# Optimization experiments

Measured on AMD Instinct MI355X. Metric: run time of the kernel, lower is better.

Reference implementation:

```python
import jax, jax.numpy as jnp
import numpy as np
from jax import lax

B, C, H, W = 16, 384, 28, 28
HEADS = 8


def _ln(x, g, b):
    mu = jnp.mean(x, axis=-1, keepdims=True)
    var = jnp.var(x, axis=-1, keepdims=True)
    return (x - mu) * lax.rsqrt(var + 1e-5) * g + b


def setup_inputs() -> dict:
    key = jax.random.key(0)
    ks = jax.random.split(key, 8)
    s = 0.02
    return {
        "cls_token": jax.random.normal(ks[0], (B, 1, C), dtype=jnp.float32),
        "x": jax.random.normal(ks[1], (B, C, H, W), dtype=jnp.float32),
        "conv_w": jax.random.normal(ks[2], (C, 1, 3, 3), dtype=jnp.float32) * s,
        "conv_b": jnp.zeros((C,), jnp.float32),
        "ln1_g": jnp.ones((C,), jnp.float32),
        "ln1_b": jnp.zeros((C,), jnp.float32),
        "qkv_w": jax.random.normal(ks[3], (3 * C, C), dtype=jnp.float32) * s,
        "proj_w": jax.random.normal(ks[4], (C, C), dtype=jnp.float32) * s,
        "proj_b": jnp.zeros((C,), jnp.float32),
        "ln2_g": jnp.ones((C,), jnp.float32),
        "ln2_b": jnp.zeros((C,), jnp.float32),
        "fc1_w": jax.random.normal(ks[5], (4 * C, C), dtype=jnp.float32) * s,
        "fc1_b": jnp.zeros((4 * C,), jnp.float32),
        "fc2_w": jax.random.normal(ks[6], (C, 4 * C), dtype=jnp.float32) * s,
        "fc2_b": jnp.zeros((C,), jnp.float32),
    }


def reference(cls_token, x, conv_w, conv_b, ln1_g, ln1_b, qkv_w, proj_w, proj_b,
              ln2_g, ln2_b, fc1_w, fc1_b, fc2_w, fc2_b):
    Bv, Cv, Hv, Wv = x.shape
    h = HEADS
    d = Cv // h
    # depthwise 3x3 positional conv (groups=dim), residual add
    pe = lax.conv_general_dilated(
        x, conv_w, window_strides=(1, 1), padding="SAME",
        feature_group_count=Cv,
        dimension_numbers=("NCHW", "OIHW", "NCHW")) + conv_b[None, :, None, None]
    x = x + pe
    x_patch = x.reshape(Bv, Cv, Hv * Wv).transpose(0, 2, 1)  # [B, HW, C]
    xc = jnp.concatenate([cls_token, x_patch], axis=1)       # [B, N, C]
    N = xc.shape[1]

    # --- Attention with inline global_attn stats (first-call / int sentinel path) ---
    y = _ln(xc, ln1_g, ln1_b)
    qkv = (y @ qkv_w.T).reshape(Bv, N, 3, h, d)
    q = qkv[:, :, 0].transpose(0, 2, 1, 3)  # [B, h, N, d]
    k = qkv[:, :, 1].transpose(0, 2, 1, 3)
    v = qkv[:, :, 2].transpose(0, 2, 1, 3)
    scale = d ** -0.5
    attn = jax.nn.softmax(jnp.einsum("bhnd,bhmd->bhnm", q, k) * scale, axis=-1)
    # per-token global attention statistic: mean over heads of cls row (excl. cls)
    global_attn = jnp.mean(attn[:, :, 0, 1:], axis=1)  # [B, N-1]
    o = jnp.einsum("bhnm,bhmd->bhnd", attn, v).transpose(0, 2, 1, 3).reshape(Bv, N, Cv)
    xc = xc + (o @ proj_w.T + proj_b)

    # --- MLP (GELU exact, matching torch nn.GELU default) ---
    y2 = _ln(xc, ln2_g, ln2_b)
    m = jax.nn.gelu(y2 @ fc1_w.T + fc1_b, approximate=False) @ fc2_w.T + fc2_b
    xc = xc + m

    cls_out = xc[:, :1]                                            # [B, 1, C]
    x_out = xc[:, 1:].transpose(0, 2, 1).reshape(Bv, Cv, Hv, Wv)    # [B, C, H, W]
    return cls_out, x_out, global_attn
```

## Files before the change

kernel.cpp:

```cpp
#include <hip/hip_runtime.h>
#include <hip/hip_bf16.h>

#define DI __device__ __forceinline__

typedef __attribute__((ext_vector_type(4))) float f32x4;
typedef __attribute__((ext_vector_type(8))) short bf16x8;
typedef __attribute__((ext_vector_type(4))) short bf16x4;

static constexpr int CB = 16;
static constexpr int CC = 384;
static constexpr int CH = 28, CW = 28;
static constexpr int CD = 48;
static constexpr int CN = 785;
static constexpr int CM = CB * CN;
static constexpr int C3 = 3 * CC;
static constexpr int CF = 4 * CC;
static constexpr int HW = CH * CW;
static constexpr int NP = 832;

DI short f2b(float f) {
  __hip_bfloat16 h = __float2bfloat16(f);
  return *reinterpret_cast<short*>(&h);
}
DI float b2f(short s) {
  union { unsigned u; float f; } x;
  x.u = ((unsigned)(unsigned short)s) << 16;
  return x.f;
}

DI void gload16(const short* g, short* l) {
  __builtin_amdgcn_global_load_lds((const __attribute__((address_space(1))) void*)g,
                                   (__attribute__((address_space(3))) void*)l, 16, 0, 0);
}

__global__ void k_misc(const float* __restrict__ cls, float* __restrict__ xc,
                       float* __restrict__ ga) {
  const int gid = blockIdx.x * 256 + threadIdx.x;
  if (gid < CB * HW) ga[gid] = 0.f;
  if (gid < CB * CC) {
    const int b = gid / CC, c = gid % CC;
    xc[((size_t)b * CN) * CC + c] = cls[gid];
  }
}

__global__ void k_wconv(const float* __restrict__ s0, const float* __restrict__ s1,
                        const float* __restrict__ s2, const float* __restrict__ s3,
                        short* __restrict__ dst) {
  const int gid = (blockIdx.x * 256 + threadIdx.x) * 4;
  if (gid >= 1769472) return;
  const float* s; int off;
  if (gid < 442368)       { s = s0; off = gid; }
  else if (gid < 589824)  { s = s1; off = gid - 442368; }
  else if (gid < 1179648) { s = s2; off = gid - 589824; }
  else                    { s = s3; off = gid - 1179648; }
  f32x4 v = *(const f32x4*)(s + off);
  bf16x4 o;
#pragma unroll
  for (int i = 0; i < 4; i++) o[i] = f2b(v[i]);
  *(bf16x4*)(dst + gid) = o;
}

__global__ __launch_bounds__(256) void k_conv_t(const float* __restrict__ x,
                                                const float* __restrict__ cw,
                                                const float* __restrict__ cb,
                                                float* __restrict__ xc) {
  __shared__ float T[64][65];
  __shared__ float Wc[64 * 9];
  __shared__ float Cbs[64];
  const int b = blockIdx.z;
  const int cc = blockIdx.y * 64;
  const int hw0 = blockIdx.x * 64;
  const int t = threadIdx.x;
  const int hwi = t & 63, ci0 = t >> 6;
  const int hw = hw0 + hwi;
  const int yy = hw / CW, xx = hw % CW;
  const int ci2 = t & 63, hb2 = t >> 6;

  for (int i = t; i < 64 * 9; i += 256) Wc[i] = cw[cc * 9 + i];
  if (t < 64) Cbs[t] = cb[cc + t];
  __syncthreads();
  if (hw < HW) {
#pragma unroll
    for (int j = 0; j < 16; j++) {
      const int cl = ci0 * 16 + j;
      const float* xp = x + ((size_t)(b * CC + cc + cl)) * HW;
      float acc = Cbs[cl];
      const float center = xp[yy * CW + xx];
#pragma unroll
      for (int ky = 0; ky < 3; ky++) {
        const int iy = yy + ky - 1;
        if (iy < 0 || iy >= CH) continue;
#pragma unroll
        for (int kx = 0; kx < 3; kx++) {
          const int ix = xx + kx - 1;
          if (ix < 0 || ix >= CW) continue;
          acc += Wc[cl * 9 + ky * 3 + kx] * xp[iy * CW + ix];
        }
      }
      T[cl][hwi] = center + acc;
    }
  }
  __syncthreads();
#pragma unroll
  for (int j = 0; j < 16; j++) {
    const int hwl = hb2 + j * 4;
    if (hw0 + hwl < HW)
      xc[((size_t)b * CN + 1 + hw0 + hwl) * CC + cc + ci2] = T[ci2][hwl];
  }
}

__global__ __launch_bounds__(256) void k_ln(const float* __restrict__ xin,
                                            const float* __restrict__ g,
                                            const float* __restrict__ bta,
                                            short* __restrict__ y, int Mtot) {
  const int row = blockIdx.x * 4 + (threadIdx.x >> 6);
  const int l = threadIdx.x & 63;
  if (row >= Mtot) return;
  const float* xr = xin + (size_t)row * CC;
  float v[6], s = 0.f, ss = 0.f;
#pragma unroll
  for (int i = 0; i < 6; i++) {
    v[i] = xr[l + i * 64];
    s += v[i];
    ss += v[i] * v[i];
  }
#pragma unroll
  for (int m = 1; m < 64; m <<= 1) { s += __shfl_xor(s, m); ss += __shfl_xor(ss, m); }
  const float mu = s * (1.f / CC);
  const float var = ss * (1.f / CC) - mu * mu;
  const float r = rsqrtf(var + 1e-5f);
#pragma unroll
  for (int i = 0; i < 6; i++) {
    const int c = l + i * 64;
    y[(size_t)row * CC + c] = f2b((v[i] - mu) * r * g[c] + bta[c]);
  }
}

template <int BM, int DOGELU, int DORES, int DOBIAS, int OUTBF>
__global__ __launch_bounds__(256) void k_gemm(const short* __restrict__ A,
                                              const short* __restrict__ W,
                                              const float* __restrict__ bias,
                                              const float* __restrict__ resid,
                                              void* __restrict__ out_,
                                              int M, int N, int K) {
  constexpr int MI = BM / 32;
  constexpr int ACALLS = BM / 64;
  __shared__ short As[2 * BM * 32];
  __shared__ short Bs[2 * 128 * 32];
  const int bm = blockIdx.x * BM, bn = blockIdx.y * 128;
  const int t = threadIdx.x, w = t >> 6, l = t & 63, g = l >> 4, li = l & 15;
  const int wm = (w >> 1) * (BM / 2), wn = (w & 1) * 64;

  const int srow = l >> 2;
  const int scol = (l & 3) * 8;
  const short* aSrc[ACALLS]; int aOff[ACALLS];
#pragma unroll
  for (int j = 0; j < ACALLS; j++) {
    int arow = bm + w * (BM / 4) + j * 16 + srow; if (arow > M - 1) arow = M - 1;
    aSrc[j] = A + (size_t)arow * K + scol;
    aOff[j] = (w * (BM / 4) + j * 16) * 32;
  }
  const short* bSrc[2]; int bOff[2];
#pragma unroll
  for (int j = 0; j < 2; j++) {
    const int brow = bn + w * 32 + j * 16 + srow;
    bSrc[j] = W + (size_t)brow * K + scol;
    bOff[j] = (w * 32 + j * 16) * 32;
  }

  auto stage = [&](int buf, int kt) {
    const int ko = kt * 32;
#pragma unroll
    for (int j = 0; j < ACALLS; j++)
      gload16(aSrc[j] + ko, &As[buf * (BM * 32)] + aOff[j]);
#pragma unroll
    for (int j = 0; j < 2; j++)
      gload16(bSrc[j] + ko, &Bs[buf * (128 * 32)] + bOff[j]);
  };

  f32x4 acc[MI][4] = {};
  const int nkt = K / 32;
  stage(0, 0);
  __syncthreads();
  int cur = 0;
  for (int kt = 0; kt < nkt; kt++) {
    if (kt + 1 < nkt) stage(cur ^ 1, kt + 1);
    const short* Ab = &As[cur * (BM * 32)];
    const short* Bb = &Bs[cur * (128 * 32)];
    bf16x8 af[MI], bf[4];
#pragma unroll
    for (int mi = 0; mi < MI; mi++)
      af[mi] = *(const bf16x8*)&Ab[(wm + mi * 16 + li) * 32 + g * 8];
#pragma unroll
    for (int ni = 0; ni < 4; ni++)
      bf[ni] = *(const bf16x8*)&Bb[(wn + ni * 16 + li) * 32 + g * 8];
#pragma unroll
    for (int mi = 0; mi < MI; mi++)
#pragma unroll
      for (int ni = 0; ni < 4; ni++)
        acc[mi][ni] = __builtin_amdgcn_mfma_f32_16x16x32_bf16(af[mi], bf[ni], acc[mi][ni], 0, 0, 0);
    __syncthreads();
    cur ^= 1;
  }

#pragma unroll
  for (int mi = 0; mi < MI; mi++)
#pragma unroll
    for (int ni = 0; ni < 4; ni++) {
      const int col = bn + wn + ni * 16 + li;
      float bv = 0.f;
      if constexpr (DOBIAS) bv = bias[col];
#pragma unroll
      for (int r = 0; r < 4; r++) {
        const int row = bm + wm + mi * 16 + g * 4 + r;
        if (row < M) {
          float v = acc[mi][ni][r] + bv;
          if constexpr (DOGELU) v = 0.5f * v * (1.f + erff(v * 0.7071067811865475f));
          if constexpr (DORES) v += resid[(size_t)row * N + col];
          if constexpr (OUTBF)
            ((short*)out_)[(size_t)row * N + col] = f2b(v);
          else
            ((float*)out_)[(size_t)row * N + col] = v;
        }
      }
    }
}

__global__ __launch_bounds__(256) void k_vt(const short* __restrict__ qkv,
                                            short* __restrict__ vt) {
  __shared__ short Tl[48 * 71];
  const int n0 = blockIdx.x * 64;
  const int bh = blockIdx.y;
  const int b = bh >> 3, h = bh & 7;
  const int t = threadIdx.x;
  const size_t bbase = (size_t)b * CN;
#pragma unroll
  for (int it = 0; it < 2; it++) {
    const int gi = t + it * 256;
    if (gi < 384) {
      const int nrel = gi / 6, dg = gi % 6;
      const int n = n0 + nrel;
      bf16x8 val = {};
      if (n < CN)
        val = *(const bf16x8*)(qkv + (bbase + n) * C3 + 2 * CC + h * CD + dg * 8);
#pragma unroll
      for (int i = 0; i < 8; i++) Tl[(dg * 8 + i) * 71 + nrel] = val[i];
    }
  }
  __syncthreads();
#pragma unroll
  for (int it = 0; it < 2; it++) {
    const int gj = t + it * 256;
    if (gj < 384) {
      const int d = gj >> 3, ng = gj & 7;
      bf16x8 v;
#pragma unroll
      for (int i = 0; i < 8; i++) v[i] = Tl[d * 71 + ng * 8 + i];
      *(bf16x8*)(vt + ((size_t)bh * CD + d) * NP + n0 + ng * 8) = v;
    }
  }
}

__global__ __launch_bounds__(256) void k_attn(const short* __restrict__ qkv,
                                              const short* __restrict__ vt,
                                              short* __restrict__ o) {
  __shared__ short Ks[64 * 48];
  __shared__ short Vs[48 * 64];
  const int f = blockIdx.x;
  const int xslot = f & 7, grp = f >> 3;
  const int bh = xslot + 8 * (grp & 15);
  const int qt = grp >> 4;
  const int b = bh >> 3, h = bh & 7;
  const int q0 = qt * 64;
  const int t = threadIdx.x, w = t >> 6, l = t & 63, g = l >> 4, li = l & 15;
  const size_t bbase = (size_t)b * CN;

  const int qrow = q0 + w * 16 + li;
  const int qr = qrow > CN - 1 ? CN - 1 : qrow;
  const short* qb = qkv + (bbase + qr) * C3 + h * CD;
  bf16x8 qf0 = *(const bf16x8*)(qb + g * 8);
  bf16x8 qf1 = {};
  if (g < 2) qf1 = *(const bf16x8*)(qb + 32 + g * 8);

  float mr = -1e30f, ls = 0.f;
  f32x4 oa[3] = {};
  const float scale = 0.14433756729740643f;

  const int krow0 = t / 6, kcg0 = t % 6;
  const int krow1 = (t + 256) / 6, kcg1 = (t + 256) % 6;
  const int vd0 = t >> 3, vkvg0 = t & 7;
  const int vd1 = (t + 256) >> 3, vkvg1 = (t + 256) & 7;
  const short* kbase = qkv + bbase * C3 + CC + h * CD;
  const short* vbase = vt + (size_t)bh * CD * NP;

  bf16x8 kr0 = {}, kr1 = {}, vr0 = {}, vr1 = {};
  kr0 = *(const bf16x8*)(kbase + (size_t)min(krow0, CN - 1) * C3 + kcg0 * 8);
  vr0 = *(const bf16x8*)(vbase + vd0 * NP + vkvg0 * 8);
  if (t < 128) {
    kr1 = *(const bf16x8*)(kbase + (size_t)min(krow1, CN - 1) * C3 + kcg1 * 8);
    vr1 = *(const bf16x8*)(vbase + vd1 * NP + vkvg1 * 8);
  }

  for (int kt = 0; kt < 13; kt++) {
    const int kv0 = kt * 64;
    __syncthreads();
    *(bf16x8*)((char*)Ks + ((krow0 * 96 + kcg0 * 16) ^ ((krow0 & 7) << 4))) = kr0;
    *(bf16x8*)((char*)Vs + ((vd0 * 128 + vkvg0 * 16) ^ ((vd0 & 7) << 4))) = vr0;
    if (t < 128) {
      *(bf16x8*)((char*)Ks + ((krow1 * 96 + kcg1 * 16) ^ ((krow1 & 7) << 4))) = kr1;
      *(bf16x8*)((char*)Vs + ((vd1 * 128 + vkvg1 * 16) ^ ((vd1 & 7) << 4))) = vr1;
    }
    __syncthreads();
    if (kt < 12) {
      const int kn = kv0 + 64;
      kr0 = *(const bf16x8*)(kbase + (size_t)min(kn + krow0, CN - 1) * C3 + kcg0 * 8);
      vr0 = *(const bf16x8*)(vbase + vd0 * NP + kn + vkvg0 * 8);
      if (t < 128) {
        kr1 = *(const bf16x8*)(kbase + (size_t)min(kn + krow1, CN - 1) * C3 + kcg1 * 8);
        vr1 = *(const bf16x8*)(vbase + vd1 * NP + kn + vkvg1 * 8);
      }
    }

    f32x4 s[4];
    __builtin_amdgcn_s_setprio(1);
#pragma unroll
    for (int ni = 0; ni < 4; ni++) {
      const int krw = ni * 16 + li;
      const int sw = (krw & 7) << 4;
      bf16x8 kf0 = *(const bf16x8*)((char*)Ks + ((krw * 96 + g * 16) ^ sw));
      bf16x8 kf1 = {};
      if (g < 2) kf1 = *(const bf16x8*)((char*)Ks + ((krw * 96 + 64 + g * 16) ^ sw));
      f32x4 acc = {};
      acc = __builtin_amdgcn_mfma_f32_16x16x32_bf16(kf0, qf0, acc, 0, 0, 0);
      acc = __builtin_amdgcn_mfma_f32_16x16x32_bf16(kf1, qf1, acc, 0, 0, 0);
      s[ni] = acc;
    }
    __builtin_amdgcn_s_setprio(0);

    float mt = -1e30f;
#pragma unroll
    for (int ni = 0; ni < 4; ni++)
#pragma unroll
      for (int r = 0; r < 4; r++) {
        const int kva = kv0 + ni * 16 + g * 4 + r;
        const float v = (kva < CN) ? s[ni][r] * scale : -1e30f;
        s[ni][r] = v;
        mt = fmaxf(mt, v);
      }
    mt = fmaxf(mt, __shfl_xor(mt, 16));
    mt = fmaxf(mt, __shfl_xor(mt, 32));
    const float mn = fmaxf(mr, mt);
    const float al = __expf(mr - mn);
    mr = mn;
    float ps = 0.f;
#pragma unroll
    for (int ni = 0; ni < 4; ni++)
#pragma unroll
      for (int r = 0; r < 4; r++) {
        const float p = __expf(s[ni][r] - mn);
        s[ni][r] = p;
        ps += p;
      }
    ps += __shfl_xor(ps, 16);
    ps += __shfl_xor(ps, 32);
    ls = ls * al + ps;

    const int sb = (l & 48) + ((l & 48) >> 2);
    float ar[4];
#pragma unroll
    for (int r = 0; r < 4; r++) ar[r] = __shfl(al, sb + r);
#pragma unroll
    for (int d = 0; d < 3; d++)
#pragma unroll
      for (int r = 0; r < 4; r++) oa[d][r] *= ar[r];

    bf16x8 pa[2];
#pragma unroll
    for (int ks = 0; ks < 2; ks++)
#pragma unroll
      for (int i = 0; i < 8; i++)
        pa[ks][i] = f2b(i < 4 ? s[2 * ks][i] : s[2 * ks + 1][i - 4]);

    __builtin_amdgcn_s_setprio(1);
#pragma unroll
    for (int d = 0; d < 3; d++) {
      const int drow = d * 16 + li;
      const int sw = (drow & 7) << 4;
#pragma unroll
      for (int ks = 0; ks < 2; ks++) {
        bf16x4 lo = *(const bf16x4*)((char*)Vs + ((drow * 128 + ks * 64 + g * 8) ^ sw));
        bf16x4 hi = *(const bf16x4*)((char*)Vs + ((drow * 128 + ks * 64 + 32 + g * 8) ^ sw));
        bf16x8 vb;
#pragma unroll
        for (int i = 0; i < 4; i++) { vb[i] = lo[i]; vb[4 + i] = hi[i]; }
        oa[d] = __builtin_amdgcn_mfma_f32_16x16x32_bf16(pa[ks], vb, oa[d], 0, 0, 0);
      }
    }
    __builtin_amdgcn_s_setprio(0);
  }

  const int sb = (l & 48) + ((l & 48) >> 2);
  float lr[4];
#pragma unroll
  for (int r = 0; r < 4; r++) lr[r] = __shfl(ls, sb + r);
#pragma unroll
  for (int d = 0; d < 3; d++)
#pragma unroll
    for (int r = 0; r < 4; r++) {
      const int n = q0 + w * 16 + g * 4 + r;
      if (n < CN)
        o[(bbase + n) * CC + h * CD + d * 16 + li] = f2b(oa[d][r] / lr[r]);
    }
}

__global__ __launch_bounds__(256) void k_gattn(const short* __restrict__ qkv,
                                               float* __restrict__ ga) {
  const int b = blockIdx.x >> 3, h = blockIdx.x & 7;
  __shared__ float red[4];
  const int t = threadIdx.x;
  const size_t bbase = (size_t)b * CN;
  const short* q0 = qkv + bbase * C3 + h * CD;
  float qv[CD];
#pragma unroll
  for (int i = 0; i < CD; i++) qv[i] = b2f(q0[i]);
  float lg[4], ev[4];
  float lmax = -1e30f;
#pragma unroll
  for (int j = 0; j < 4; j++) {
    const int m = t + j * 256;
    if (m < CN) {
      const short* kr = qkv + (bbase + m) * C3 + CC + h * CD;
      float acc = 0.f;
#pragma unroll
      for (int i = 0; i < CD; i++) acc += qv[i] * b2f(kr[i]);
      lg[j] = acc * 0.14433756729740643f;
      lmax = fmaxf(lmax, lg[j]);
    } else lg[j] = -1e30f;
  }
  for (int msk = 1; msk < 64; msk <<= 1) lmax = fmaxf(lmax, __shfl_xor(lmax, msk));
  if ((t & 63) == 0) red[t >> 6] = lmax;
  __syncthreads();
  lmax = fmaxf(fmaxf(red[0], red[1]), fmaxf(red[2], red[3]));
  __syncthreads();
  float es = 0.f;
#pragma unroll
  for (int j = 0; j < 4; j++) {
    ev[j] = (t + j * 256 < CN) ? __expf(lg[j] - lmax) : 0.f;
    es += ev[j];
  }
  for (int msk = 1; msk < 64; msk <<= 1) es += __shfl_xor(es, msk);
  if ((t & 63) == 0) red[t >> 6] = es;
  __syncthreads();
  es = red[0] + red[1] + red[2] + red[3];
  const float inv = 0.125f / es;
#pragma unroll
  for (int j = 0; j < 4; j++) {
    const int m = t + j * 256;
    if (m >= 1 && m < CN) atomicAdd(&ga[b * HW + m - 1], ev[j] * inv);
  }
}

__global__ __launch_bounds__(256) void k_out(const float* __restrict__ xc,
                                             float* __restrict__ outp) {
  const int b = blockIdx.y, tile = blockIdx.x, t = threadIdx.x;
  if (tile == 78) {
    for (int i = t; i < CC; i += 256)
      outp[b * CC + i] = xc[((size_t)b * CN) * CC + i];
    return;
  }
  __shared__ float T[64][65];
  const int ct = tile / 13, ht = tile % 13;
  const int c0 = ct * 64, hw0 = ht * 64;
  const int ci = t & 63, hb = t >> 6;
  for (int j = 0; j < 16; j++) {
    const int hwl = hb + j * 4;
    if (hw0 + hwl < HW)
      T[ci][hwl] = xc[((size_t)b * CN + 1 + hw0 + hwl) * CC + c0 + ci];
  }
  __syncthreads();
  const int hi = t & 63, cb2 = t >> 6;
  float* xo = outp + CB * CC;
  for (int j = 0; j < 16; j++) {
    const int cl = cb2 + j * 4;
    if (hw0 + hi < HW)
      xo[((size_t)(b * CC + c0 + cl)) * HW + hw0 + hi] = T[cl][hi];
  }
}

extern "C" void kernel_launch(void* const* d_in, const int* in_sizes, int n_in,
                              void* d_out, int out_size, void* d_ws, size_t ws_size,
                              hipStream_t stream) {
  const float* cls    = (const float*)d_in[0];
  const float* x      = (const float*)d_in[1];
  const float* conv_w = (const float*)d_in[2];
  const float* conv_b = (const float*)d_in[3];
  const float* ln1_g  = (const float*)d_in[4];
  const float* ln1_b  = (const float*)d_in[5];
  const float* qkv_w  = (const float*)d_in[6];
  const float* proj_w = (const float*)d_in[7];
  const float* proj_b = (const float*)d_in[8];
  const float* ln2_g  = (const float*)d_in[9];
  const float* ln2_b  = (const float*)d_in[10];
  const float* fc1_w  = (const float*)d_in[11];
  const float* fc1_b  = (const float*)d_in[12];
  const float* fc2_w  = (const float*)d_in[13];
  const float* fc2_b  = (const float*)d_in[14];

  float* outf = (float*)d_out;
  float* ga = outf + (size_t)CB * CC + (size_t)CB * CC * HW;
  short* vtb = (short*)(outf + CB * CC);

  char* ws = (char*)d_ws;
  float* xc   = (float*)ws;
  short* y    = (short*)(ws + 19292160ULL);
  short* qkvb = (short*)(ws + 28938240ULL);
  short* o    = (short*)(ws + 57876480ULL);
  short* m1   = (short*)(ws + 28938240ULL);
  short* wbuf = (short*)(ws + 67522560ULL);
  short* qkv_wb = wbuf;
  short* proj_wb = wbuf + 442368;
  short* fc1_wb  = wbuf + 589824;
  short* fc2_wb  = wbuf + 1179648;

  const int thr = 256;
  k_misc<<<49, thr, 0, stream>>>(cls, xc, ga);
  k_wconv<<<1728, thr, 0, stream>>>(qkv_w, proj_w, fc1_w, fc2_w, wbuf);
  k_conv_t<<<dim3(13, 6, CB), thr, 0, stream>>>(x, conv_w, conv_b, xc);
  k_ln<<<CM / 4, thr, 0, stream>>>(xc, ln1_g, ln1_b, y, CM);
  k_gemm<128, 0, 0, 0, 1><<<dim3(99, C3 / 128), thr, 0, stream>>>(
      y, qkv_wb, nullptr, nullptr, qkvb, CM, C3, CC);
  k_vt<<<dim3(13, CB * 8), thr, 0, stream>>>(qkvb, vtb);
  k_attn<<<1664, thr, 0, stream>>>(qkvb, vtb, o);
  k_gattn<<<CB * 8, thr, 0, stream>>>(qkvb, ga);
  k_gemm<64, 0, 1, 1, 0><<<dim3(197, CC / 128), thr, 0, stream>>>(
      o, proj_wb, proj_b, xc, xc, CM, CC, CC);
  k_ln<<<CM / 4, thr, 0, stream>>>(xc, ln2_g, ln2_b, y, CM);
  k_gemm<128, 1, 0, 1, 1><<<dim3(99, CF / 128), thr, 0, stream>>>(
      y, fc1_wb, fc1_b, nullptr, m1, CM, CF, CC);
  k_gemm<64, 0, 1, 1, 0><<<dim3(197, CC / 128), thr, 0, stream>>>(
      m1, fc2_wb, fc2_b, xc, xc, CM, CC, CF);
  k_out<<<dim3(79, CB), thr, 0, stream>>>(xc, outf);
}
```

Measured before the change: 370.2 us.

## Triple-buffer GEMM LDS staging with explicit vmcnt waits; restructure depthwise conv loads

The GEMM kernel moves from double to triple buffering of the A/B tiles in shared memory. It keeps two k-tiles of global-to-LDS loads in flight and uses explicit s_waitcnt vmcnt counts plus raw barriers instead of __syncthreads, so load latency is hidden behind MFMA work. The depthwise conv kernel precomputes clamped neighbour offsets and masks, then processes two channels per iteration with branch-free loads. The costs are more LDS per block, which may lower occupancy, and hand-tuned vmcnt values that must match the exact number of loads issued per stage.

New measurement: 351.0 us. 1.05x faster.

```diff
diff --git a/kernel.cpp b/kernel.cpp
--- a/kernel.cpp
+++ b/kernel.cpp
@@ -80,24 +80,34 @@
   if (t < 64) Cbs[t] = cb[cc + t];
   __syncthreads();
   if (hw < HW) {
-#pragma unroll
-    for (int j = 0; j < 16; j++) {
-      const int cl = ci0 * 16 + j;
-      const float* xp = x + ((size_t)(b * CC + cc + cl)) * HW;
-      float acc = Cbs[cl];
-      const float center = xp[yy * CW + xx];
-#pragma unroll
-      for (int ky = 0; ky < 3; ky++) {
-        const int iy = yy + ky - 1;
-        if (iy < 0 || iy >= CH) continue;
-#pragma unroll
-        for (int kx = 0; kx < 3; kx++) {
-          const int ix = xx + kx - 1;
-          if (ix < 0 || ix >= CW) continue;
-          acc += Wc[cl * 9 + ky * 3 + kx] * xp[iy * CW + ix];
-        }
-      }
-      T[cl][hwi] = center + acc;
+    const int ctr = yy * CW + xx;
+    int off9[9]; float mk9[9];
+#pragma unroll
+    for (int ky = 0; ky < 3; ky++)
+#pragma unroll
+      for (int kx = 0; kx < 3; kx++) {
+        const int iy = yy + ky - 1, ix = xx + kx - 1;
+        const bool v = (iy >= 0 && iy < CH && ix >= 0 && ix < CW);
+        off9[ky * 3 + kx] = v ? iy * CW + ix : ctr;
+        mk9[ky * 3 + kx] = v ? 1.f : 0.f;
+      }
+#pragma unroll
+    for (int j = 0; j < 16; j += 2) {
+      const int cl0 = ci0 * 16 + j;
+      const float* xp0 = x + ((size_t)(b * CC + cc + cl0)) * HW;
+      const float* xp1 = xp0 + HW;
+      float t0[9], t1[9];
+#pragma unroll
+      for (int q = 0; q < 9; q++) { t0[q] = xp0[off9[q]]; t1[q] = xp1[off9[q]]; }
+      const float c0 = xp0[ctr], c1 = xp1[ctr];
+      float a0 = Cbs[cl0], a1 = Cbs[cl0 + 1];
+#pragma unroll
+      for (int q = 0; q < 9; q++) {
+        a0 += Wc[cl0 * 9 + q] * (t0[q] * mk9[q]);
+        a1 += Wc[(cl0 + 1) * 9 + q] * (t1[q] * mk9[q]);
+      }
+      T[cl0][hwi] = c0 + a0;
+      T[cl0 + 1][hwi] = c1 + a1;
     }
   }
   __syncthreads();
@@ -145,8 +155,9 @@
                                               int M, int N, int K) {
   constexpr int MI = BM / 32;
   constexpr int ACALLS = BM / 64;
-  __shared__ short As[2 * BM * 32];
-  __shared__ short Bs[2 * 128 * 32];
+  constexpr int ASZ = BM * 32, BSZ = 128 * 32;
+  __shared__ short As[3 * ASZ];
+  __shared__ short Bs[3 * BSZ];
   const int bm = blockIdx.x * BM, bn = blockIdx.y * 128;
   const int t = threadIdx.x, w = t >> 6, l = t & 63, g = l >> 4, li = l & 15;
   const int wm = (w >> 1) * (BM / 2), wn = (w & 1) * 64;
@@ -172,21 +183,34 @@
     const int ko = kt * 32;
 #pragma unroll
     for (int j = 0; j < ACALLS; j++)
-      gload16(aSrc[j] + ko, &As[buf * (BM * 32)] + aOff[j]);
+      gload16(aSrc[j] + ko, &As[buf * ASZ] + aOff[j]);
 #pragma unroll
     for (int j = 0; j < 2; j++)
-      gload16(bSrc[j] + ko, &Bs[buf * (128 * 32)] + bOff[j]);
+      gload16(bSrc[j] + ko, &Bs[buf * BSZ] + bOff[j]);
   };
 
   f32x4 acc[MI][4] = {};
   const int nkt = K / 32;
   stage(0, 0);
-  __syncthreads();
+  stage(1, 1);
   int cur = 0;
   for (int kt = 0; kt < nkt; kt++) {
-    if (kt + 1 < nkt) stage(cur ^ 1, kt + 1);
-    const short* Ab = &As[cur * (BM * 32)];
-    const short* Bb = &Bs[cur * (128 * 32)];
+    if (kt + 2 < nkt) {
+      int nb = cur + 2; if (nb >= 3) nb -= 3;
+      stage(nb, kt + 2);
+      if constexpr (BM == 128) asm volatile("s_waitcnt vmcnt(8)" ::: "memory");
+      else                     asm volatile("s_waitcnt vmcnt(6)" ::: "memory");
+    } else if (kt + 2 == nkt) {
+      if constexpr (BM == 128) asm volatile("s_waitcnt vmcnt(4)" ::: "memory");
+      else                     asm volatile("s_waitcnt vmcnt(3)" ::: "memory");
+    } else {
+      asm volatile("s_waitcnt vmcnt(0)" ::: "memory");
+    }
+    __builtin_amdgcn_sched_barrier(0);
+    __builtin_amdgcn_s_barrier();
+
+    const short* Ab = &As[cur * ASZ];
+    const short* Bb = &Bs[cur * BSZ];
     bf16x8 af[MI], bf[4];
 #pragma unroll
     for (int mi = 0; mi < MI; mi++)
@@ -199,8 +223,11 @@
 #pragma unroll
       for (int ni = 0; ni < 4; ni++)
         acc[mi][ni] = __builtin_amdgcn_mfma_f32_16x16x32_bf16(af[mi], bf[ni], acc[mi][ni], 0, 0, 0);
-    __syncthreads();
-    cur ^= 1;
+
+    asm volatile("s_waitcnt lgkmcnt(0)" ::: "memory");
+    __builtin_amdgcn_sched_barrier(0);
+    __builtin_amdgcn_s_barrier();
+    cur = (cur == 2) ? 0 : cur + 1;
   }
 
 #pragma unroll
```
